# Performance work log

Hardware: AMD Instinct MI355X
Metric: run time of the kernel (lower is better)

## Reference

```python
import jax, jax.numpy as jnp
import numpy as np

H = 1024      # hidden_size
NH = 16       # attention heads
DH = H // NH  # head dim
B, S = 4, 2048
EPS = 1e-12


def setup_inputs() -> dict:
    key = jax.random.key(0)
    ks = jax.random.split(key, 9)
    sc = 1.0 / np.sqrt(H)
    inp = {
        "input_tensor": jax.random.normal(ks[0], (B, S, H), dtype=jnp.float32),
        "Wq": jax.random.normal(ks[1], (H, H), dtype=jnp.float32) * sc,
        "bq": jnp.zeros((H,), jnp.float32),
        "Wk": jax.random.normal(ks[2], (H, H), dtype=jnp.float32) * sc,
        "bk": jnp.zeros((H,), jnp.float32),
        "Wv": jax.random.normal(ks[3], (H, H), dtype=jnp.float32) * sc,
        "bv": jnp.zeros((H,), jnp.float32),
        "Wo": jax.random.normal(ks[4], (H, H), dtype=jnp.float32) * sc,
        "bo": jnp.zeros((H,), jnp.float32),
        "gamma": jnp.ones((H,), jnp.float32),
        "beta": jnp.zeros((H,), jnp.float32),
    }
    return inp


def _heads(x):
    # [B,S,H] -> [B,NH,S,DH]
    b, s, _ = x.shape
    return x.reshape(b, s, NH, DH).transpose(0, 2, 1, 3)


def reference(input_tensor, Wq, bq, Wk, bk, Wv, bv, Wo, bo, gamma, beta):
    q = _heads(input_tensor @ Wq.T + bq)
    k = _heads(input_tensor @ Wk.T + bk)
    v = _heads(input_tensor @ Wv.T + bv)
    scores = jnp.einsum("bhqd,bhkd->bhqk", q, k) / jnp.sqrt(jnp.float32(DH))
    probs = jax.nn.softmax(scores, axis=-1)  # dropout p=0 -> identity
    ctx = jnp.einsum("bhqk,bhkd->bhqd", probs, v)
    ctx = ctx.transpose(0, 2, 1, 3).reshape(input_tensor.shape)  # [B,S,H]
    h = ctx @ Wo.T + bo
    x = h + input_tensor
    u = jnp.mean(x, axis=-1, keepdims=True)
    s2 = jnp.mean((x - u) ** 2, axis=-1, keepdims=True)
    xn = (x - u) / jnp.sqrt(s2 + EPS)
    return gamma * xn + beta
```

## Files before the change

### kernel.cpp

```cpp
#include <hip/hip_runtime.h>
#include <math.h>

#define H   1024
#define NH  16
#define DH  64
#define BB  4
#define SS  2048
#define M_ROWS (BB*SS)
#define EPS 1e-12f
#define QSCALE 0.18033688011112042f

typedef __attribute__((ext_vector_type(4))) float f32x4;
typedef __attribute__((ext_vector_type(8))) short bf16x8;
typedef const __attribute__((address_space(1))) void* as1cvp;
typedef __attribute__((address_space(3))) void*       as3vp;
typedef const __attribute__((address_space(1))) ushort* as1u;
typedef __attribute__((address_space(3))) ushort*       as3u;

__device__ __forceinline__ unsigned short f2bf(float f) {
    union { float f; unsigned u; } x; x.f = f;
    unsigned r = x.u + 0x7fffu + ((x.u >> 16) & 1u);
    return (unsigned short)(r >> 16);
}
__device__ __forceinline__ unsigned pk2bf(float lo, float hi) {
    return __builtin_amdgcn_perm(__float_as_uint(hi), __float_as_uint(lo), 0x07060302u);
}

__global__ __launch_bounds__(256)
void cvt_all(const float4* __restrict__ x,
             const float4* __restrict__ wq, const float4* __restrict__ wk,
             const float4* __restrict__ wv, const float4* __restrict__ wo,
             ushort4* __restrict__ xb, ushort4* __restrict__ wqb,
             ushort4* __restrict__ wkb, ushort4* __restrict__ wvb,
             ushort4* __restrict__ wob)
{
    int id = blockIdx.x * 256 + threadIdx.x;
    const float4* src; ushort4* dst; int off;
    if (id < 2097152) { src = x; dst = xb; off = id; }
    else {
        int t = id - 2097152, wsel = t >> 18;
        off = t & 262143;
        src = wsel == 0 ? wq : wsel == 1 ? wk : wsel == 2 ? wv : wo;
        dst = wsel == 0 ? wqb : wsel == 1 ? wkb : wsel == 2 ? wvb : wob;
    }
    float4 v = src[off];
    ushort4 o; o.x = f2bf(v.x); o.y = f2bf(v.y); o.z = f2bf(v.z); o.w = f2bf(v.w);
    dst[off] = o;
}

#define STAGE_QKV(ofs, k0)                                                              \
    __builtin_amdgcn_global_load_lds((as1cvp)(gA + gAr0 + (k0)),                        \
                                     (as3vp)(lds + (ofs) + dA0), 16, 0, 0);             \
    __builtin_amdgcn_global_load_lds((as1cvp)(gA + gAr1 + (k0)),                        \
                                     (as3vp)(lds + (ofs) + dA1), 16, 0, 0);             \
    __builtin_amdgcn_global_load_lds((as1cvp)(gB + gBr0 + (k0)),                        \
                                     (as3vp)(lds + (ofs) + 4096 + dA0), 16, 0, 0);      \
    __builtin_amdgcn_global_load_lds((as1cvp)(gB + gBr1 + (k0)),                        \
                                     (as3vp)(lds + (ofs) + 4096 + dA1), 16, 0, 0);

__device__ __forceinline__ void gemm_core_128(const ushort* __restrict__ A,
                                              const ushort* __restrict__ Wt,
                                              ushort* ldsP,
                                              int row0, int col0, int K,
                                              f32x4 (&acc)[4][4])
{
    const int tid = threadIdx.x, lane = tid & 63, w = tid >> 6;
    const int wr = w >> 1, wc = w & 1, l15 = lane & 15, quad = lane >> 4;
    const int lr = lane >> 2, kc = lane & 3;
    const int qs  = kc ^ ((lr >> 1) & 3);
    const int qsw = (quad ^ ((l15 >> 1) & 3)) * 8;

    const as1u gA = (as1u)A;
    const as1u gB = (as1u)Wt;
    as3u lds = (as3u)ldsP;

    const int ra = (w * 2) * 16 + lr;
    const int rb = ra + 16;
    const size_t gAr0 = (size_t)(row0 + ra) * K + qs * 8;
    const size_t gAr1 = (size_t)(row0 + rb) * K + qs * 8;
    const size_t gBr0 = (size_t)(col0 + ra) * K + qs * 8;
    const size_t gBr1 = (size_t)(col0 + rb) * K + qs * 8;
    const int dA0 = (w * 2 + 0) * 512;
    const int dA1 = (w * 2 + 1) * 512;

    STAGE_QKV(0, 0);
    STAGE_QKV(8192, 32);

    int cur = 0;
    for (int k0 = 0; k0 < K; k0 += 32) {
        if (k0 + 32 < K) asm volatile("s_waitcnt vmcnt(4)" ::: "memory");
        else             asm volatile("s_waitcnt vmcnt(0)" ::: "memory");
        __builtin_amdgcn_s_barrier();

        int nxt2 = cur + 16384; if (nxt2 >= 24576) nxt2 -= 24576;
        if (k0 + 64 < K) { STAGE_QKV(nxt2, k0 + 64); }

        const ushort* AsP = ldsP + cur;
        const ushort* BsP = ldsP + cur + 4096;
        bf16x8 af[4], bfr[4];
        #pragma unroll
        for (int rt = 0; rt < 4; ++rt)
            af[rt] = *(const bf16x8*)&AsP[(wr * 64 + rt * 16 + l15) * 32 + qsw];
        #pragma unroll
        for (int ct = 0; ct < 4; ++ct)
            bfr[ct] = *(const bf16x8*)&BsP[(wc * 64 + ct * 16 + l15) * 32 + qsw];
        #pragma unroll
        for (int rt = 0; rt < 4; ++rt)
            #pragma unroll
            for (int ct = 0; ct < 4; ++ct)
                acc[rt][ct] = __builtin_amdgcn_mfma_f32_16x16x32_bf16(af[rt], bfr[ct], acc[rt][ct], 0, 0, 0);

        cur += 8192; if (cur == 24576) cur = 0;
    }
}

__global__ __launch_bounds__(256, 3)
void qkv_gemm(const ushort* __restrict__ xb,
              const ushort* __restrict__ Wqb, const ushort* __restrict__ Wkb,
              const ushort* __restrict__ Wvb,
              const float* __restrict__ bq, const float* __restrict__ bk,
              const float* __restrict__ bv,
              ushort* __restrict__ Qb, ushort* __restrict__ Kb, ushort* __restrict__ Vt)
{
    __shared__ __align__(16) ushort Ls[3 * 8192];
    const int lin = blockIdx.x;
    const int swz = (lin & 7) * 192 + (lin >> 3);
    const int z   = swz >> 9;
    const int rem = swz & 511;
    const int row0 = (rem >> 3) * 128;
    const int col0 = (rem & 7) * 128;

    const ushort* Wt  = z == 0 ? Wqb : z == 1 ? Wkb : Wvb;
    const float* bias = z == 0 ? bq  : z == 1 ? bk  : bv;

    f32x4 acc[4][4];
    #pragma unroll
    for (int i = 0; i < 4; ++i)
        #pragma unroll
        for (int j = 0; j < 4; ++j)
            acc[i][j] = (f32x4){0.f, 0.f, 0.f, 0.f};

    gemm_core_128(xb, Wt, Ls, row0, col0, H, acc);

    const int tid = threadIdx.x, lane = tid & 63, w = tid >> 6;
    const int wr = w >> 1, wc = w & 1, l15 = lane & 15, quad = lane >> 4;

    #pragma unroll
    for (int rt = 0; rt < 4; ++rt) {
        const int r0g = row0 + wr * 64 + rt * 16 + quad * 4;
        #pragma unroll
        for (int ct = 0; ct < 4; ++ct) {
            const int c = col0 + wc * 64 + ct * 16 + l15;
            const float bs = bias[c];
            if (z == 0) {
                #pragma unroll
                for (int i = 0; i < 4; ++i)
                    Qb[(size_t)(r0g + i) * H + c] = f2bf((acc[rt][ct][i] + bs) * QSCALE);
            } else if (z == 1) {
                #pragma unroll
                for (int i = 0; i < 4; ++i)
                    Kb[(size_t)(r0g + i) * H + c] = f2bf(acc[rt][ct][i] + bs);
            } else {
                const int bb = r0g >> 11, s0 = r0g & 2047;
                const int hh = c >> 6, dd = c & 63;
                ushort4 o;
                o.x = f2bf(acc[rt][ct][0] + bs);
                o.y = f2bf(acc[rt][ct][1] + bs);
                o.z = f2bf(acc[rt][ct][2] + bs);
                o.w = f2bf(acc[rt][ct][3] + bs);
                *(ushort4*)&Vt[(((size_t)(bb * 16 + hh) * 64 + dd) << 11) + s0] = o;
            }
        }
    }
}

__global__ __launch_bounds__(256, 3)
void oproj_gemm(const ushort* __restrict__ ctxb, const ushort* __restrict__ Wob,
                const float* __restrict__ bo, const float* __restrict__ res,
                float* __restrict__ Xr)
{
    __shared__ __align__(16) ushort Ls[3 * 8192];
    const int lin = blockIdx.x;
    const int swz = (lin & 7) * 64 + (lin >> 3);
    const int row0 = (swz >> 3) * 128;
    const int col0 = (swz & 7) * 128;

    f32x4 acc[4][4];
    #pragma unroll
    for (int i = 0; i < 4; ++i)
        #pragma unroll
        for (int j = 0; j < 4; ++j)
            acc[i][j] = (f32x4){0.f, 0.f, 0.f, 0.f};

    gemm_core_128(ctxb, Wob, Ls, row0, col0, H, acc);

    const int tid = threadIdx.x, lane = tid & 63, w = tid >> 6;
    const int wr = w >> 1, wc = w & 1, l15 = lane & 15, quad = lane >> 4;

    #pragma unroll
    for (int rt = 0; rt < 4; ++rt) {
        const int r0g = row0 + wr * 64 + rt * 16 + quad * 4;
        #pragma unroll
        for (int ct = 0; ct < 4; ++ct) {
            const int c = col0 + wc * 64 + ct * 16 + l15;
            const float bs = bo[c];
            #pragma unroll
            for (int i = 0; i < 4; ++i) {
                size_t idx = (size_t)(r0g + i) * H + c;
                Xr[idx] = acc[rt][ct][i] + bs + res[idx];
            }
        }
    }
}

#define KTILE 64
#define NKT (SS / KTILE)

__global__ __launch_bounds__(256, 2)
void flash_attn_mfma(const ushort* __restrict__ Qb, const ushort* __restrict__ Kb,
                     const ushort* __restrict__ Vt, ushort* __restrict__ ctx)
{
    __shared__ __align__(16) ushort Ks[2][KTILE * 64];
    __shared__ __align__(16) ushort Vs[2][64 * KTILE];

    const int tid  = threadIdx.x;
    const int lane = tid & 63;
    const int w    = tid >> 6;
    const int l15  = lane & 15, quad = lane >> 4;
    const int bh   = blockIdx.x & 63;
    const int qt   = blockIdx.x >> 6;
    const int b    = bh >> 4, h = bh & 15;
    const int row0 = qt * 256 + w * 64;
    const size_t qk_base = (size_t)(b * SS) * H + h * DH;
    const size_t vt_base = (size_t)((b * 16 + h) * 64) * SS;

    const as1u gK = (const as1u)Kb;
    const as1u gV = (const as1u)Vt;

    const int srow = lane >> 3;
    const int c8   = lane & 7;
    const int sck0 = c8 ^ ((srow & 3) | (((w * 2 + 0) & 1) << 2));
    const int sck1 = c8 ^ ((srow & 3) | (((w * 2 + 1) & 1) << 2));

    const int fL = (l15 & 3) | (((l15 >> 2) & 1) << 2);
    const int fV = (l15 & 3) | (((l15 >> 3) & 1) << 2);
    const int rA = 8 * (l15 >> 2) + (l15 & 3);
    int kOff0[4], kOff1[4], vOff0[4], vOff1[4];
    #pragma unroll
    for (int ct = 0; ct < 4; ++ct) {
        const int r = rA + (ct & 1) * 4 + (ct >> 1) * 32;
        kOff0[ct] = r * 64 + ((quad ^ fL) * 8);
        kOff1[ct] = r * 64 + (((4 | quad) ^ fL) * 8);
    }
    #pragma unroll
    for (int dt = 0; dt < 4; ++dt) {
        const int rv = dt * 16 + l15;
        vOff0[dt] = rv * 64 + ((quad ^ fV) * 8);
        vOff1[dt] = rv * 64 + (((4 | quad) ^ fV) * 8);
    }

    bf16x8 aq[4][2];
    #pragma unroll
    for (int g = 0; g < 4; ++g) {
        const size_t qrow = qk_base + (size_t)(row0 + g * 16 + l15) * H;
        aq[g][0] = *(const bf16x8*)&Qb[qrow + quad * 8];
        aq[g][1] = *(const bf16x8*)&Qb[qrow + 32 + quad * 8];
    }

    union { unsigned u[4]; bf16x8 v; } ONES;
    #pragma unroll
    for (int i = 0; i < 4; ++i) ONES.u[i] = 0x3F803F80u;

    f32x4 acc_l[4];
    f32x4 o[4][4];
    #pragma unroll
    for (int g = 0; g < 4; ++g) {
        acc_l[g] = (f32x4){0.f, 0.f, 0.f, 0.f};
        #pragma unroll
        for (int dt = 0; dt < 4; ++dt) o[g][dt] = (f32x4){0.f, 0.f, 0.f, 0.f};
    }

    const as1u gK0 = gK + qk_base + (size_t)(w * 16 + srow) * H;
    const as1u gV0 = gV + vt_base + (size_t)(w * 16 + srow) * SS;

    __builtin_amdgcn_global_load_lds((as1cvp)(gK0 + sck0 * 8),
                                     (as3vp)(&Ks[0][(w * 16) * 64]), 16, 0, 0);
    __builtin_amdgcn_global_load_lds((as1cvp)(gK0 + (size_t)8 * H + sck1 * 8),
                                     (as3vp)(&Ks[0][(w * 16 + 8) * 64]), 16, 0, 0);
    __builtin_amdgcn_global_load_lds((as1cvp)(gV0 + sck0 * 8),
                                     (as3vp)(&Vs[0][(w * 16) * 64]), 16, 0, 0);
    __builtin_amdgcn_global_load_lds((as1cvp)(gV0 + (size_t)8 * SS + sck1 * 8),
                                     (as3vp)(&Vs[0][(w * 16 + 8) * 64]), 16, 0, 0);

    for (int kt = 0; kt < NKT; ++kt) {
        __syncthreads();

        if (kt + 1 < NKT) {
            const int j0 = (kt + 1) * KTILE;
            const int nb = (kt + 1) & 1;
            __builtin_amdgcn_global_load_lds((as1cvp)(gK0 + (size_t)j0 * H + sck0 * 8),
                                             (as3vp)(&Ks[nb][(w * 16) * 64]), 16, 0, 0);
            __builtin_amdgcn_global_load_lds((as1cvp)(gK0 + (size_t)(j0 + 8) * H + sck1 * 8),
                                             (as3vp)(&Ks[nb][(w * 16 + 8) * 64]), 16, 0, 0);
            __builtin_amdgcn_global_load_lds((as1cvp)(gV0 + j0 + sck0 * 8),
                                             (as3vp)(&Vs[nb][(w * 16) * 64]), 16, 0, 0);
            __builtin_amdgcn_global_load_lds((as1cvp)(gV0 + (size_t)8 * SS + j0 + sck1 * 8),
                                             (as3vp)(&Vs[nb][(w * 16 + 8) * 64]), 16, 0, 0);
        }

        const ushort* Ktile = Ks[kt & 1];
        const ushort* Vtile = Vs[kt & 1];

        f32x4 s[4][4];
        __builtin_amdgcn_s_setprio(1);
        #pragma unroll
        for (int ct = 0; ct < 4; ++ct) {
            const bf16x8 k0 = *(const bf16x8*)&Ktile[kOff0[ct]];
            const bf16x8 k1 = *(const bf16x8*)&Ktile[kOff1[ct]];
            #pragma unroll
            for (int g = 0; g < 4; ++g) {
                f32x4 z = (f32x4){0.f, 0.f, 0.f, 0.f};
                z = __builtin_amdgcn_mfma_f32_16x16x32_bf16(k0, aq[g][0], z, 0, 0, 0);
                z = __builtin_amdgcn_mfma_f32_16x16x32_bf16(k1, aq[g][1], z, 0, 0, 0);
                s[g][ct] = z;
            }
        }
        __builtin_amdgcn_s_setprio(0);

        union { unsigned u[4]; bf16x8 v; } A[4][2];
        #pragma unroll
        for (int g = 0; g < 4; ++g) {
            #pragma unroll
            for (int ct = 0; ct < 4; ++ct) {
                const float p0 = __builtin_amdgcn_exp2f(s[g][ct][0]);
                const float p1 = __builtin_amdgcn_exp2f(s[g][ct][1]);
                const float p2 = __builtin_amdgcn_exp2f(s[g][ct][2]);
                const float p3 = __builtin_amdgcn_exp2f(s[g][ct][3]);
                A[g][ct >> 1].u[(ct & 1) * 2 + 0] = pk2bf(p0, p1);
                A[g][ct >> 1].u[(ct & 1) * 2 + 1] = pk2bf(p2, p3);
            }
        }

        __builtin_amdgcn_s_setprio(1);
        #pragma unroll
        for (int g = 0; g < 4; ++g) {
            acc_l[g] = __builtin_amdgcn_mfma_f32_16x16x32_bf16(A[g][0].v, ONES.v, acc_l[g], 0, 0, 0);
            acc_l[g] = __builtin_amdgcn_mfma_f32_16x16x32_bf16(A[g][1].v, ONES.v, acc_l[g], 0, 0, 0);
        }
        #pragma unroll
        for (int dt = 0; dt < 4; ++dt) {
            const bf16x8 v0 = *(const bf16x8*)&Vtile[vOff0[dt]];
            const bf16x8 v1 = *(const bf16x8*)&Vtile[vOff1[dt]];
            #pragma unroll
            for (int g = 0; g < 4; ++g) {
                o[g][dt] = __builtin_amdgcn_mfma_f32_16x16x32_bf16(A[g][0].v, v0, o[g][dt], 0, 0, 0);
                o[g][dt] = __builtin_amdgcn_mfma_f32_16x16x32_bf16(A[g][1].v, v1, o[g][dt], 0, 0, 0);
            }
        }
        __builtin_amdgcn_s_setprio(0);
    }

    #pragma unroll
    for (int g = 0; g < 4; ++g) {
        #pragma unroll
        for (int i = 0; i < 4; ++i) {
            const float inv = 1.f / acc_l[g][i];
            const int r = row0 + g * 16 + quad * 4 + i;
            #pragma unroll
            for (int dt = 0; dt < 4; ++dt)
                ctx[qk_base + (size_t)r * H + dt * 16 + l15] = f2bf(o[g][dt][i] * inv);
        }
    }
}

__global__ __launch_bounds__(256)
void ln_kernel(const float* __restrict__ Xr, const float* __restrict__ gamma,
               const float* __restrict__ beta, float* __restrict__ out)
{
    __shared__ float red[4], red2[4];
    const int row = blockIdx.x;
    const int tid = threadIdx.x;
    const int lane = tid & 63, w = tid >> 6;
    const float4 v = ((const float4*)(Xr + (size_t)row * H))[tid];
    float s  = v.x + v.y + v.z + v.w;
    float ss = v.x * v.x + v.y * v.y + v.z * v.z + v.w * v.w;
    #pragma unroll
    for (int d = 1; d < 64; d <<= 1) {
        s  += __shfl_xor(s, d);
        ss += __shfl_xor(ss, d);
    }
    if (lane == 0) { red[w] = s; red2[w] = ss; }
    __syncthreads();
    s  = red[0]  + red[1]  + red[2]  + red[3];
    ss = red2[0] + red2[1] + red2[2] + red2[3];
    const float mean = s * (1.f / H);
    const float var  = ss * (1.f / H) - mean * mean;
    const float rstd = rsqrtf(var + EPS);
    const float4 g  = ((const float4*)gamma)[tid];
    const float4 be = ((const float4*)beta)[tid];
    float4 o;
    o.x = g.x * (v.x - mean) * rstd + be.x;
    o.y = g.y * (v.y - mean) * rstd + be.y;
    o.z = g.z * (v.z - mean) * rstd + be.z;
    o.w = g.w * (v.w - mean) * rstd + be.w;
    ((float4*)(out + (size_t)row * H))[tid] = o;
}

extern "C" void kernel_launch(void* const* d_in, const int* in_sizes, int n_in,
                              void* d_out, int out_size, void* d_ws, size_t ws_size,
                              hipStream_t stream)
{
    const float* x     = (const float*)d_in[0];
    const float* Wq    = (const float*)d_in[1];
    const float* bq    = (const float*)d_in[2];
    const float* Wk    = (const float*)d_in[3];
    const float* bk    = (const float*)d_in[4];
    const float* Wv    = (const float*)d_in[5];
    const float* bv    = (const float*)d_in[6];
    const float* Wo    = (const float*)d_in[7];
    const float* bo    = (const float*)d_in[8];
    const float* gamma = (const float*)d_in[9];
    const float* beta  = (const float*)d_in[10];

    char* ws = (char*)d_ws;
    ushort* xb  = (ushort*)(ws);
    ushort* Wqb = (ushort*)(ws + (size_t)(16 << 20));
    ushort* Wkb = (ushort*)(ws + (size_t)(18 << 20));
    ushort* Wvb = (ushort*)(ws + (size_t)(20 << 20));
    ushort* Wob = (ushort*)(ws + (size_t)(22 << 20));
    ushort* Qb  = (ushort*)(ws + (size_t)(24 << 20));
    ushort* Kb  = (ushort*)(ws + (size_t)(40 << 20));
    ushort* Vt  = (ushort*)(ws + (size_t)(56 << 20));
    float*  Xr  = (float*) (ws + (size_t)(40 << 20));

    cvt_all<<<12288, 256, 0, stream>>>((const float4*)x, (const float4*)Wq, (const float4*)Wk,
                                       (const float4*)Wv, (const float4*)Wo,
                                       (ushort4*)xb, (ushort4*)Wqb, (ushort4*)Wkb,
                                       (ushort4*)Wvb, (ushort4*)Wob);

    qkv_gemm<<<1536, 256, 0, stream>>>(
        xb, Wqb, Wkb, Wvb, bq, bk, bv, Qb, Kb, Vt);

    flash_attn_mfma<<<BB * NH * (SS / 256), 256, 0, stream>>>(Qb, Kb, Vt, Qb );

    oproj_gemm<<<512, 256, 0, stream>>>(Qb, Wob, bo, x, Xr);

    ln_kernel<<<M_ROWS, 256, 0, stream>>>(Xr, gamma, beta, (float*)d_out);
}
```

Measured before the change: 275.1 us.

## Load GEMM weight fragments directly from global into registers, bypassing LDS

The shared GEMM core no longer stages the weight (B) tile through LDS. Each lane loads its own B fragments straight from global memory into registers, double-buffered one k-step ahead, while only the activation (A) tile stays on the LDS triple-buffer path. This halves the LDS footprint and removes the LDS reads for B, which could allow higher occupancy. In exchange, B reads are no longer shared through LDS: the two waves that share a column tile each fetch it separately from global/L2, and register pressure rises. The wait counts were adjusted to cover the extra in-flight loads.

```diff
diff --git a/kernel.cpp b/kernel.cpp
--- a/kernel.cpp
+++ b/kernel.cpp
@@ -48,15 +48,11 @@
     dst[off] = o;
 }
 
-#define STAGE_QKV(ofs, k0)                                                              \
+#define STAGE_A(ofs, k0)                                                                \
     __builtin_amdgcn_global_load_lds((as1cvp)(gA + gAr0 + (k0)),                        \
                                      (as3vp)(lds + (ofs) + dA0), 16, 0, 0);             \
     __builtin_amdgcn_global_load_lds((as1cvp)(gA + gAr1 + (k0)),                        \
-                                     (as3vp)(lds + (ofs) + dA1), 16, 0, 0);             \
-    __builtin_amdgcn_global_load_lds((as1cvp)(gB + gBr0 + (k0)),                        \
-                                     (as3vp)(lds + (ofs) + 4096 + dA0), 16, 0, 0);      \
-    __builtin_amdgcn_global_load_lds((as1cvp)(gB + gBr1 + (k0)),                        \
-                                     (as3vp)(lds + (ofs) + 4096 + dA1), 16, 0, 0);
+                                     (as3vp)(lds + (ofs) + dA1), 16, 0, 0);
 
 __device__ __forceinline__ void gemm_core_128(const ushort* __restrict__ A,
                                               const ushort* __restrict__ Wt,
@@ -74,43 +70,55 @@
     const as1u gB = (as1u)Wt;
     as3u lds = (as3u)ldsP;
 
-    const int ra = (w * 2) * 16 + lr;
+    const int ra = w * 32 + lr;
     const int rb = ra + 16;
     const size_t gAr0 = (size_t)(row0 + ra) * K + qs * 8;
     const size_t gAr1 = (size_t)(row0 + rb) * K + qs * 8;
-    const size_t gBr0 = (size_t)(col0 + ra) * K + qs * 8;
-    const size_t gBr1 = (size_t)(col0 + rb) * K + qs * 8;
     const int dA0 = (w * 2 + 0) * 512;
     const int dA1 = (w * 2 + 1) * 512;
 
-    STAGE_QKV(0, 0);
-    STAGE_QKV(8192, 32);
+    int bOff[4];
+    #pragma unroll
+    for (int ct = 0; ct < 4; ++ct)
+        bOff[ct] = (col0 + wc * 64 + ct * 16 + l15) * K + quad * 8;
+
+    STAGE_A(0, 0);
+    STAGE_A(4096, 32);
+    bf16x8 bcur[4], bnxt[4];
+    #pragma unroll
+    for (int ct = 0; ct < 4; ++ct) bcur[ct] = *(const bf16x8*)&gB[bOff[ct]];
+    #pragma unroll
+    for (int ct = 0; ct < 4; ++ct) bnxt[ct] = bcur[ct];
 
     int cur = 0;
     for (int k0 = 0; k0 < K; k0 += 32) {
-        if (k0 + 32 < K) asm volatile("s_waitcnt vmcnt(4)" ::: "memory");
+        if (k0 + 32 < K) asm volatile("s_waitcnt vmcnt(6)" ::: "memory");
         else             asm volatile("s_waitcnt vmcnt(0)" ::: "memory");
         __builtin_amdgcn_s_barrier();
 
-        int nxt2 = cur + 16384; if (nxt2 >= 24576) nxt2 -= 24576;
-        if (k0 + 64 < K) { STAGE_QKV(nxt2, k0 + 64); }
+        int nxt2 = cur + 8192; if (nxt2 >= 12288) nxt2 -= 12288;
+        if (k0 + 64 < K) { STAGE_A(nxt2, k0 + 64); }
+        if (k0 + 32 < K) {
+            #pragma unroll
+            for (int ct = 0; ct < 4; ++ct)
+                bnxt[ct] = *(const bf16x8*)&gB[bOff[ct] + k0 + 32];
+        }
 
         const ushort* AsP = ldsP + cur;
-        const ushort* BsP = ldsP + cur + 4096;
-        bf16x8 af[4], bfr[4];
+        bf16x8 af[4];
         #pragma unroll
         for (int rt = 0; rt < 4; ++rt)
             af[rt] = *(const bf16x8*)&AsP[(wr * 64 + rt * 16 + l15) * 32 + qsw];
         #pragma unroll
-        for (int ct = 0; ct < 4; ++ct)
-            bfr[ct] = *(const bf16x8*)&BsP[(wc * 64 + ct * 16 + l15) * 32 + qsw];
-        #pragma unroll
         for (int rt = 0; rt < 4; ++rt)
             #pragma unroll
             for (int ct = 0; ct < 4; ++ct)
-                acc[rt][ct] = __builtin_amdgcn_mfma_f32_16x16x32_bf16(af[rt], bfr[ct], acc[rt][ct], 0, 0, 0);
-
-        cur += 8192; if (cur == 24576) cur = 0;
+                acc[rt][ct] = __builtin_amdgcn_mfma_f32_16x16x32_bf16(af[rt], bcur[ct], acc[rt][ct], 0, 0, 0);
+
+        #pragma unroll
+        for (int ct = 0; ct < 4; ++ct) bcur[ct] = bnxt[ct];
+
+        cur += 4096; if (cur == 12288) cur = 0;
     }
 }
 
@@ -122,7 +130,7 @@
               const float* __restrict__ bv,
               ushort* __restrict__ Qb, ushort* __restrict__ Kb, ushort* __restrict__ Vt)
 {
-    __shared__ __align__(16) ushort Ls[3 * 8192];
+    __shared__ __align__(16) ushort Ls[3 * 4096];
     const int lin = blockIdx.x;
     const int swz = (lin & 7) * 192 + (lin >> 3);
     const int z   = swz >> 9;
@@ -179,7 +187,7 @@
                 const float* __restrict__ bo, const float* __restrict__ res,
                 float* __restrict__ Xr)
 {
-    __shared__ __align__(16) ushort Ls[3 * 8192];
+    __shared__ __align__(16) ushort Ls[3 * 4096];
     const int lin = blockIdx.x;
     const int swz = (lin & 7) * 64 + (lin >> 3);
     const int row0 = (swz >> 3) * 128;
```

New measurement: 334.9 us. 1.22x slower.

## Enlarge GEMM tiles to 128x256 with 512 threads and 64-deep K stages

Applied to the files above, without the earlier changes.

The QKV and output-projection GEMMs now use 128x256 output tiles computed by 8 waves (512 threads) instead of 128x128 tiles with 4 waves. Each pipeline stage loads a 64-wide K slice, split into two 32-wide halves, and the triple-buffered LDS grows to 144 KB per block. The aim is more reuse of each loaded A tile across columns and half as many barriers per K. In exchange, fewer blocks are launched (768 and 256), occupancy per CU drops, and the 256-block output projection may leave some CUs idle.

```diff
diff --git a/kernel.cpp b/kernel.cpp
--- a/kernel.cpp
+++ b/kernel.cpp
@@ -48,73 +48,72 @@
     dst[off] = o;
 }
 
-#define STAGE_QKV(ofs, k0)                                                              \
-    __builtin_amdgcn_global_load_lds((as1cvp)(gA + gAr0 + (k0)),                        \
-                                     (as3vp)(lds + (ofs) + dA0), 16, 0, 0);             \
-    __builtin_amdgcn_global_load_lds((as1cvp)(gA + gAr1 + (k0)),                        \
-                                     (as3vp)(lds + (ofs) + dA1), 16, 0, 0);             \
-    __builtin_amdgcn_global_load_lds((as1cvp)(gB + gBr0 + (k0)),                        \
-                                     (as3vp)(lds + (ofs) + 4096 + dA0), 16, 0, 0);      \
-    __builtin_amdgcn_global_load_lds((as1cvp)(gB + gBr1 + (k0)),                        \
-                                     (as3vp)(lds + (ofs) + 4096 + dA1), 16, 0, 0);
-
-__device__ __forceinline__ void gemm_core_128(const ushort* __restrict__ A,
+#define GL(gsrc, ldst) __builtin_amdgcn_global_load_lds((as1cvp)(gsrc), (as3vp)(ldst), 16, 0, 0)
+#define STAGE_T(ofs, kt)                                                        \
+    GL(gA + aOff  + (kt) * 64,      lds + (ofs) + w512);                        \
+    GL(gA + aOff  + (kt) * 64 + 32, lds + (ofs) + 4096 + w512);                 \
+    GL(gB + bOff0 + (kt) * 64,      lds + (ofs) + 8192 + w1024);                \
+    GL(gB + bOff0 + (kt) * 64 + 32, lds + (ofs) + 16384 + w1024);               \
+    GL(gB + bOff1 + (kt) * 64,      lds + (ofs) + 8192 + w1024 + 512);          \
+    GL(gB + bOff1 + (kt) * 64 + 32, lds + (ofs) + 16384 + w1024 + 512);
+
+__device__ __forceinline__ void gemm_core_256(const ushort* __restrict__ A,
                                               const ushort* __restrict__ Wt,
                                               ushort* ldsP,
                                               int row0, int col0, int K,
                                               f32x4 (&acc)[4][4])
 {
     const int tid = threadIdx.x, lane = tid & 63, w = tid >> 6;
-    const int wr = w >> 1, wc = w & 1, l15 = lane & 15, quad = lane >> 4;
-    const int lr = lane >> 2, kc = lane & 3;
-    const int qs  = kc ^ ((lr >> 1) & 3);
+    const int wr = w >> 2, wc = w & 3, l15 = lane & 15, quad = lane >> 4;
     const int qsw = (quad ^ ((l15 >> 1) & 3)) * 8;
+
+    const int sc = (lane & 3) ^ ((lane >> 3) & 3);
 
     const as1u gA = (as1u)A;
     const as1u gB = (as1u)Wt;
     as3u lds = (as3u)ldsP;
 
-    const int ra = (w * 2) * 16 + lr;
-    const int rb = ra + 16;
-    const size_t gAr0 = (size_t)(row0 + ra) * K + qs * 8;
-    const size_t gAr1 = (size_t)(row0 + rb) * K + qs * 8;
-    const size_t gBr0 = (size_t)(col0 + ra) * K + qs * 8;
-    const size_t gBr1 = (size_t)(col0 + rb) * K + qs * 8;
-    const int dA0 = (w * 2 + 0) * 512;
-    const int dA1 = (w * 2 + 1) * 512;
-
-    STAGE_QKV(0, 0);
-    STAGE_QKV(8192, 32);
+    const size_t aOff  = (size_t)(row0 + w * 16 + (lane >> 2)) * K + sc * 8;
+    const size_t bOff0 = (size_t)(col0 + w * 32 + (lane >> 2)) * K + sc * 8;
+    const size_t bOff1 = (size_t)(col0 + w * 32 + 16 + (lane >> 2)) * K + sc * 8;
+    const int w512 = w * 512, w1024 = w * 1024;
+
+    const int NT = K >> 6;
+    STAGE_T(0, 0);
+    STAGE_T(24576, 1);
 
     int cur = 0;
-    for (int k0 = 0; k0 < K; k0 += 32) {
-        if (k0 + 32 < K) asm volatile("s_waitcnt vmcnt(4)" ::: "memory");
-        else             asm volatile("s_waitcnt vmcnt(0)" ::: "memory");
+    for (int t = 0; t < NT; ++t) {
+        if (t + 1 < NT) asm volatile("s_waitcnt vmcnt(6)" ::: "memory");
+        else            asm volatile("s_waitcnt vmcnt(0)" ::: "memory");
         __builtin_amdgcn_s_barrier();
 
-        int nxt2 = cur + 16384; if (nxt2 >= 24576) nxt2 -= 24576;
-        if (k0 + 64 < K) { STAGE_QKV(nxt2, k0 + 64); }
-
-        const ushort* AsP = ldsP + cur;
-        const ushort* BsP = ldsP + cur + 4096;
-        bf16x8 af[4], bfr[4];
-        #pragma unroll
-        for (int rt = 0; rt < 4; ++rt)
-            af[rt] = *(const bf16x8*)&AsP[(wr * 64 + rt * 16 + l15) * 32 + qsw];
-        #pragma unroll
-        for (int ct = 0; ct < 4; ++ct)
-            bfr[ct] = *(const bf16x8*)&BsP[(wc * 64 + ct * 16 + l15) * 32 + qsw];
-        #pragma unroll
-        for (int rt = 0; rt < 4; ++rt)
+        int nxt2 = cur + 49152; if (nxt2 >= 73728) nxt2 -= 73728;
+        if (t + 2 < NT) { STAGE_T(nxt2, t + 2); }
+
+        const ushort* base = ldsP + cur;
+        #pragma unroll
+        for (int h = 0; h < 2; ++h) {
+            const ushort* Ah = base + h * 4096;
+            const ushort* Bh = base + 8192 + h * 8192;
+            bf16x8 af[4], bfr[4];
+            #pragma unroll
+            for (int rt = 0; rt < 4; ++rt)
+                af[rt] = *(const bf16x8*)&Ah[(wr * 64 + rt * 16 + l15) * 32 + qsw];
             #pragma unroll
             for (int ct = 0; ct < 4; ++ct)
-                acc[rt][ct] = __builtin_amdgcn_mfma_f32_16x16x32_bf16(af[rt], bfr[ct], acc[rt][ct], 0, 0, 0);
-
-        cur += 8192; if (cur == 24576) cur = 0;
-    }
-}
-
-__global__ __launch_bounds__(256, 3)
+                bfr[ct] = *(const bf16x8*)&Bh[(wc * 64 + ct * 16 + l15) * 32 + qsw];
+            #pragma unroll
+            for (int rt = 0; rt < 4; ++rt)
+                #pragma unroll
+                for (int ct = 0; ct < 4; ++ct)
+                    acc[rt][ct] = __builtin_amdgcn_mfma_f32_16x16x32_bf16(af[rt], bfr[ct], acc[rt][ct], 0, 0, 0);
+        }
+        cur += 24576; if (cur == 73728) cur = 0;
+    }
+}
+
+__global__ __launch_bounds__(512, 2)
 void qkv_gemm(const ushort* __restrict__ xb,
               const ushort* __restrict__ Wqb, const ushort* __restrict__ Wkb,
               const ushort* __restrict__ Wvb,
@@ -122,13 +121,13 @@
               const float* __restrict__ bv,
               ushort* __restrict__ Qb, ushort* __restrict__ Kb, ushort* __restrict__ Vt)
 {
-    __shared__ __align__(16) ushort Ls[3 * 8192];
+    __shared__ __align__(16) ushort Ls[3 * 24576];
     const int lin = blockIdx.x;
-    const int swz = (lin & 7) * 192 + (lin >> 3);
-    const int z   = swz >> 9;
-    const int rem = swz & 511;
-    const int row0 = (rem >> 3) * 128;
-    const int col0 = (rem & 7) * 128;
+    const int swz = (lin & 7) * 96 + (lin >> 3);
+    const int z   = swz >> 8;
+    const int rem = swz & 255;
+    const int row0 = (rem >> 2) * 128;
+    const int col0 = (rem & 3) * 256;
 
     const ushort* Wt  = z == 0 ? Wqb : z == 1 ? Wkb : Wvb;
     const float* bias = z == 0 ? bq  : z == 1 ? bk  : bv;
@@ -140,10 +139,10 @@
         for (int j = 0; j < 4; ++j)
             acc[i][j] = (f32x4){0.f, 0.f, 0.f, 0.f};
 
-    gemm_core_128(xb, Wt, Ls, row0, col0, H, acc);
+    gemm_core_256(xb, Wt, Ls, row0, col0, H, acc);
 
     const int tid = threadIdx.x, lane = tid & 63, w = tid >> 6;
-    const int wr = w >> 1, wc = w & 1, l15 = lane & 15, quad = lane >> 4;
+    const int wr = w >> 2, wc = w & 3, l15 = lane & 15, quad = lane >> 4;
 
     #pragma unroll
     for (int rt = 0; rt < 4; ++rt) {
@@ -174,16 +173,16 @@
     }
 }
 
-__global__ __launch_bounds__(256, 3)
+__global__ __launch_bounds__(512, 2)
 void oproj_gemm(const ushort* __restrict__ ctxb, const ushort* __restrict__ Wob,
                 const float* __restrict__ bo, const float* __restrict__ res,
                 float* __restrict__ Xr)
 {
-    __shared__ __align__(16) ushort Ls[3 * 8192];
+    __shared__ __align__(16) ushort Ls[3 * 24576];
     const int lin = blockIdx.x;
-    const int swz = (lin & 7) * 64 + (lin >> 3);
-    const int row0 = (swz >> 3) * 128;
-    const int col0 = (swz & 7) * 128;
+    const int swz = (lin & 7) * 32 + (lin >> 3);
+    const int row0 = (swz >> 2) * 128;
+    const int col0 = (swz & 3) * 256;
 
     f32x4 acc[4][4];
     #pragma unroll
@@ -192,10 +191,10 @@
         for (int j = 0; j < 4; ++j)
             acc[i][j] = (f32x4){0.f, 0.f, 0.f, 0.f};
 
-    gemm_core_128(ctxb, Wob, Ls, row0, col0, H, acc);
+    gemm_core_256(ctxb, Wob, Ls, row0, col0, H, acc);
 
     const int tid = threadIdx.x, lane = tid & 63, w = tid >> 6;
-    const int wr = w >> 1, wc = w & 1, l15 = lane & 15, quad = lane >> 4;
+    const int wr = w >> 2, wc = w & 3, l15 = lane & 15, quad = lane >> 4;
 
     #pragma unroll
     for (int rt = 0; rt < 4; ++rt) {
@@ -438,12 +437,12 @@
                                        (ushort4*)xb, (ushort4*)Wqb, (ushort4*)Wkb,
                                        (ushort4*)Wvb, (ushort4*)Wob);
 
-    qkv_gemm<<<1536, 256, 0, stream>>>(
+    qkv_gemm<<<768, 512, 0, stream>>>(
         xb, Wqb, Wkb, Wvb, bq, bk, bv, Qb, Kb, Vt);
 
     flash_attn_mfma<<<BB * NH * (SS / 256), 256, 0, stream>>>(Qb, Kb, Vt, Qb );
 
-    oproj_gemm<<<512, 256, 0, stream>>>(Qb, Wob, bo, x, Xr);
+    oproj_gemm<<<256, 512, 0, stream>>>(Qb, Wob, bo, x, Xr);
 
     ln_kernel<<<M_ROWS, 256, 0, stream>>>(Xr, gamma, beta, (float*)d_out);
 }
```

Measured after the change: 267.7 us. 1.03x faster.
